# Kernel tuning notes

Hardware: AMD Instinct MI355X
Metric: run time of the kernel (lower is better)

## Reference

```python
import jax, jax.numpy as jnp
import numpy as np

INPUT, HIDDEN, Z = 64, 256, 32


def setup_inputs() -> dict:
    key = jax.random.key(0)
    ks = jax.random.split(key, 16)
    B, T = 256, 1024
    s = lambda fan_in: 1.0 / np.sqrt(fan_in)
    u = lambda k, shape, b: jax.random.uniform(k, shape, jnp.float32, -b, b)
    return {
        "x": jax.random.normal(ks[0], (B, T, INPUT), jnp.float32),
        "eps": jax.random.normal(ks[1], (T, B, Z), jnp.float32),
        # encoder q(z|x,h): Linear(hidden+input -> z)
        "enc_mu_W": u(ks[2], (Z, HIDDEN + INPUT), s(HIDDEN + INPUT)),
        "enc_mu_b": u(ks[3], (Z,), s(HIDDEN + INPUT)),
        "enc_sigma_W": u(ks[4], (Z, HIDDEN + INPUT), s(HIDDEN + INPUT)),
        "enc_sigma_b": u(ks[5], (Z,), s(HIDDEN + INPUT)),
        # prior p(z|h): Linear(hidden -> z) (computed but unused, as in source)
        "prior_mu_W": u(ks[6], (Z, HIDDEN), s(HIDDEN)),
        "prior_mu_b": u(ks[7], (Z,), s(HIDDEN)),
        "prior_sigma_W": u(ks[8], (Z, HIDDEN), s(HIDDEN)),
        "prior_sigma_b": u(ks[9], (Z,), s(HIDDEN)),
        # GRU(input+z -> hidden), torch layout: [3H, in], gates order r,z,n
        "W_ih": u(ks[10], (3 * HIDDEN, INPUT + Z), s(HIDDEN)),
        "W_hh": u(ks[11], (3 * HIDDEN, HIDDEN), s(HIDDEN)),
        "b_ih": u(ks[12], (3 * HIDDEN,), s(HIDDEN)),
        "b_hh": u(ks[13], (3 * HIDDEN,), s(HIDDEN)),
    }


def _vrnn(x, eps, enc_mu_W, enc_mu_b, enc_sigma_W, enc_sigma_b,
          prior_mu_W, prior_mu_b, prior_sigma_W, prior_sigma_b,
          W_ih, W_hh, b_ih, b_hh):
    B = x.shape[0]
    x_t_first = jnp.transpose(x, (1, 0, 2))  # [T, B, input]
    h0 = jnp.zeros((B, HIDDEN), x.dtype)

    def step(h, inp):
        x_t, eps_t = inp
        # prior (dead code in source, kept for parity; DCE'd by XLA)
        _p_mu = h @ prior_mu_W.T + prior_mu_b
        _p_lv = h @ prior_sigma_W.T + prior_sigma_b
        enc_in = jnp.concatenate([x_t, h], axis=1)  # [B, input+hidden]
        z_mu = enc_in @ enc_mu_W.T + enc_mu_b
        z_logvar = enc_in @ enc_sigma_W.T + enc_sigma_b
        z_t = z_mu + eps_t * jnp.exp(0.5 * z_logvar)
        gru_in = jnp.concatenate([x_t, z_t], axis=1)  # [B, input+z]
        gi = gru_in @ W_ih.T + b_ih  # [B, 3H]
        gh = h @ W_hh.T + b_hh       # [B, 3H]
        i_r, i_z, i_n = jnp.split(gi, 3, axis=1)
        h_r, h_z, h_n = jnp.split(gh, 3, axis=1)
        r = jax.nn.sigmoid(i_r + h_r)
        u = jax.nn.sigmoid(i_z + h_z)
        n = jnp.tanh(i_n + r * h_n)
        h_new = (1.0 - u) * n + u * h
        return h_new, None

    h_last, _ = jax.lax.scan(step, h0, (x_t_first, eps))
    return h_last  # [B, hidden]


def reference(x, eps, enc_mu_W, enc_mu_b, enc_sigma_W, enc_sigma_b,
              prior_mu_W, prior_mu_b, prior_sigma_W, prior_sigma_b,
              W_ih, W_hh, b_ih, b_hh):
    return _vrnn(x, eps, enc_mu_W, enc_mu_b, enc_sigma_W, enc_sigma_b,
                 prior_mu_W, prior_mu_b, prior_sigma_W, prior_sigma_b,
                 W_ih, W_hh, b_ih, b_hh)
```

## Files before the change

### kernel.cpp

```cpp
#include <hip/hip_runtime.h>
#include <stdint.h>

#define NB 256
#define TSEQ 1024
#define TT_MAX 64

#define REG_P 16
#define LDS_P 24
#define LDSTR 76

typedef _Float16 f16;
typedef _Float16 h2 __attribute__((ext_vector_type(2)));

static __device__ __forceinline__ uint32_t pkh2(float a, float b) {
  h2 v; v[0] = (f16)a; v[1] = (f16)b;
  return __builtin_bit_cast(uint32_t, v);
}

#if __has_builtin(__builtin_amdgcn_fdot2)
static __device__ __forceinline__ float dot2u(uint32_t w, uint32_t h, float c) {
  return __builtin_amdgcn_fdot2(__builtin_bit_cast(h2, w), __builtin_bit_cast(h2, h), c, false);
}
#else
static __device__ __forceinline__ float dot2u(uint32_t w, uint32_t h, float c) {
  h2 a = __builtin_bit_cast(h2, w), b = __builtin_bit_cast(h2, h);
  return c + (float)a[0] * (float)b[0] + (float)a[1] * (float)b[1];
}
#endif

#if __has_builtin(__builtin_amdgcn_rcpf)
#define RCPF(x) __builtin_amdgcn_rcpf(x)
#else
#define RCPF(x) (1.0f / (x))
#endif

static __device__ __forceinline__ float sigm(float x) {
  return RCPF(1.0f + exp2f(-1.44269504f * x));
}
static __device__ __forceinline__ float tanh_f(float x) {
  return 1.0f - 2.0f * RCPF(1.0f + exp2f(2.88539008f * x));
}

__global__ __launch_bounds__(512) void vrnn_pack(
    const float* __restrict__ W_hh, const float* __restrict__ W_ih,
    const float* __restrict__ emW, const float* __restrict__ esW,
    uint32_t* __restrict__ whr, uint32_t* __restrict__ whl,
    uint32_t* __restrict__ whs, uint32_t* __restrict__ whz,
    uint32_t* __restrict__ wep)
{
  const int t = threadIdx.x;
  const int r = t >> 1, q = t & 1;
  for (int rr = 0; rr < 3; ++rr) {
    const float* R = W_hh + (size_t)(r + rr * 256) * 256 + q * 128;
    for (int cj = 0; cj < 4; ++cj)
      for (int i = 0; i < 4; ++i) {
        int p = cj * 4 + i;
        whr[(((size_t)rr * 4 + cj) * 512 + t) * 4 + i] = pkh2(R[2 * p], R[2 * p + 1]);
      }
    for (int p = 0; p < LDS_P; ++p)
      whl[(size_t)t * LDSTR + rr * LDS_P + p] = pkh2(R[2 * (p + REG_P)], R[2 * (p + REG_P) + 1]);
    for (int m = 0; m < 3; ++m)
      for (int k = 0; k < 2; ++k)
        for (int i = 0; i < 4; ++i) {
          int p = (10 + 2 * m + k) * 4 + i;
          whs[(((size_t)m * 6 + rr * 2 + k) * 512 + t) * 4 + i] = pkh2(R[2 * p], R[2 * p + 1]);
        }
    const float* Z = W_ih + (size_t)(r + rr * 256) * 96 + 64 + q * 16;
    for (int cj = 0; cj < 2; ++cj)
      for (int i = 0; i < 4; ++i) {
        int p = cj * 4 + i;
        whz[(((size_t)rr * 2 + cj) * 512 + t) * 4 + i] = pkh2(Z[2 * p], Z[2 * p + 1]);
      }
  }
  {
    const int e = t & 63, s = t >> 6;
    const float* esrc = (e < 32) ? (emW + (size_t)e * 320 + 64)
                                 : (esW + (size_t)(e - 32) * 320 + 64);
    for (int p4 = 0; p4 < 4; ++p4)
      for (int i = 0; i < 4; ++i) {
        int pc = s * 16 + p4 * 4 + i;
        wep[((size_t)p4 * 512 + t) * 4 + i] = pkh2(esrc[2 * pc], esrc[2 * pc + 1]);
      }
  }
}

__global__ __launch_bounds__(256, 2) void vrnn_pre(
    const float* __restrict__ x, const float* __restrict__ W_ih,
    const float* __restrict__ b_ih, const float* __restrict__ b_hh,
    const float* __restrict__ emW, const float* __restrict__ emb,
    const float* __restrict__ esW, const float* __restrict__ esb,
    f16* __restrict__ gix, f16* __restrict__ zx,
    int chunk_t0, int TT, int nTT)
{
  const int tid = threadIdx.x;
  const int b  = blockIdx.x / nTT;
  const int tt = blockIdx.x % nTT;
  const int tloc0 = tt * TT;

  uint32_t wx[3][32];
  float bias[3];
  #pragma unroll
  for (int rr = 0; rr < 3; ++rr) {
    int j = tid + rr * 256;
    const float4* wr = (const float4*)(W_ih + (size_t)j * 96);
    #pragma unroll
    for (int p4 = 0; p4 < 16; ++p4) {
      float4 v = wr[p4];
      wx[rr][2 * p4]     = pkh2(v.x, v.y);
      wx[rr][2 * p4 + 1] = pkh2(v.z, v.w);
    }
    bias[rr] = b_ih[j] + (rr < 2 ? b_hh[j] : 0.0f);
  }
  uint32_t we[32]; float ebias = 0.0f;
  if (tid < 64) {
    const float* src = (tid < 32) ? (emW + (size_t)tid * 320)
                                  : (esW + (size_t)(tid - 32) * 320);
    #pragma unroll
    for (int p = 0; p < 32; ++p) we[p] = pkh2(src[2 * p], src[2 * p + 1]);
    ebias = (tid < 32) ? emb[tid] : esb[tid - 32];
  }

  __shared__ uint32_t xs[TT_MAX * 32];
  for (int idx = tid; idx < TT * 32; idx += 256) {
    int tl = idx >> 5, pk = idx & 31;
    size_t base = ((size_t)b * TSEQ + (chunk_t0 + tloc0 + tl)) * 64 + 2 * pk;
    xs[idx] = pkh2(x[base], x[base + 1]);
  }
  __syncthreads();

  for (int tl = 0; tl < TT; ++tl) {
    float a0 = bias[0], a1 = bias[1], a2 = bias[2];
    #pragma unroll
    for (int p = 0; p < 32; ++p) {
      uint32_t u = xs[tl * 32 + p];
      a0 = dot2u(wx[0][p], u, a0);
      a1 = dot2u(wx[1][p], u, a1);
      a2 = dot2u(wx[2][p], u, a2);
    }
    size_t ob = (size_t)(tloc0 + tl) * NB + b;
    f16* g = gix + ob * 768;
    g[tid] = (f16)a0; g[tid + 256] = (f16)a1; g[tid + 512] = (f16)a2;
    if (tid < 64) {
      float a3 = ebias;
      #pragma unroll
      for (int p = 0; p < 32; ++p) a3 = dot2u(we[p], xs[tl * 32 + p], a3);
      zx[ob * 64 + tid] = (f16)a3;
    }
  }
}

__global__ __launch_bounds__(512) void vrnn_rec(
    const f16* __restrict__ gix, const f16* __restrict__ zx,
    const float* __restrict__ eps,
    const uint32_t* __restrict__ whr, const uint32_t* __restrict__ whl_g,
    const uint32_t* __restrict__ whs, const uint32_t* __restrict__ whz,
    const uint32_t* __restrict__ wep_g,
    const float* __restrict__ b_hh,
    float* __restrict__ hws, float* __restrict__ out,
    int t0, int Tlen, int first, int last)
{
  const int t = threadIdx.x;
  const int b = blockIdx.x;
  const int r = t >> 1, q = t & 1;

  uint32_t wrg[3][REG_P];
  {
    const uint4* w4 = (const uint4*)whr;
    #pragma unroll
    for (int c = 0; c < 12; ++c) {
      uint4 v = w4[c * 512 + t];
      int rr = c >> 2, p4 = c & 3;
      wrg[rr][4 * p4] = v.x; wrg[rr][4 * p4 + 1] = v.y;
      wrg[rr][4 * p4 + 2] = v.z; wrg[rr][4 * p4 + 3] = v.w;
    }
  }
  uint32_t wz[3][8];
  {
    const uint4* w4 = (const uint4*)whz;
    #pragma unroll
    for (int c = 0; c < 6; ++c) {
      uint4 v = w4[c * 512 + t];
      int rr = c >> 1, p4 = c & 1;
      wz[rr][4 * p4] = v.x; wz[rr][4 * p4 + 1] = v.y;
      wz[rr][4 * p4 + 2] = v.z; wz[rr][4 * p4 + 3] = v.w;
    }
  }
  uint32_t we[16];
  {
    const uint4* w4 = (const uint4*)wep_g;
    #pragma unroll
    for (int c = 0; c < 4; ++c) {
      uint4 v = w4[c * 512 + t];
      we[4 * c] = v.x; we[4 * c + 1] = v.y; we[4 * c + 2] = v.z; we[4 * c + 3] = v.w;
    }
  }
  #pragma unroll
  for (int rr = 0; rr < 3; ++rr) {
    #pragma unroll
    for (int i = 0; i < REG_P; ++i) asm volatile("" : "+v"(wrg[rr][i]));
    #pragma unroll
    for (int i = 0; i < 8; ++i)    asm volatile("" : "+v"(wz[rr][i]));
  }
  #pragma unroll
  for (int i = 0; i < 16; ++i) asm volatile("" : "+v"(we[i]));
  const float bhn = b_hh[512 + r];

  __shared__ uint32_t lwh[512 * LDSTR];
  __shared__ __align__(16) f16 hf[2][264];
  __shared__ float encp[512];
  __shared__ uint32_t zu[16];

  {
    const uint4* src = (const uint4*)(whl_g + (size_t)t * LDSTR);
    uint4* dst = (uint4*)(lwh + (size_t)t * LDSTR);
    #pragma unroll
    for (int j = 0; j < LDSTR / 4; ++j) dst[j] = src[j];
  }

  const int hwidx = r + ((r >> 7) << 3);
  float hm = 0.0f;
  if (!q) {
    hm = first ? 0.0f : hws[b * 256 + r];
    hf[0][hwidx] = (f16)hm;
  }
  __syncthreads();

  float pf_g0 = 0.0f, pf_g1 = 0.0f, pf_g2 = 0.0f;
  if (!q) {
    const f16* gp0 = gix + (size_t)b * 768;
    pf_g0 = (float)gp0[r]; pf_g1 = (float)gp0[r + 256]; pf_g2 = (float)gp0[r + 512];
  }
  float pf_zm = 0.0f, pf_zl = 0.0f, pf_ep = 0.0f;
  if (t < 32) {
    const f16* zp = zx + (size_t)b * 64;
    pf_zm = (float)zp[t]; pf_zl = (float)zp[32 + t];
    pf_ep = eps[((size_t)t0 * NB + b) * 32 + t];
  }

  const int s = t >> 6;
  const int abase = 4 * s + (s >= 4 ? 1 : 0);
  const int bq = q ? 17 : 0;
  const uint32_t* myl = lwh + (size_t)t * LDSTR;
  const uint4* whs4 = (const uint4*)whs;

  uint4 sbuf[6];
  #pragma unroll
  for (int j = 0; j < 6; ++j) sbuf[j] = whs4[j * 512 + t];
  __builtin_amdgcn_sched_barrier(0);

  for (int tl = 0; tl < Tlen; ++tl) {
    const int cur = tl & 1, nxt = cur ^ 1;
    const uint4* hu4 = (const uint4*)&hf[cur][0];

    float ep_ = 0.0f;
    #pragma unroll
    for (int p4 = 0; p4 < 4; ++p4) {
      uint4 u4 = hu4[abase + p4];
      ep_ = dot2u(we[4 * p4],     u4.x, ep_);
      ep_ = dot2u(we[4 * p4 + 1], u4.y, ep_);
      ep_ = dot2u(we[4 * p4 + 2], u4.z, ep_);
      ep_ = dot2u(we[4 * p4 + 3], u4.w, ep_);
    }
    encp[t] = ep_;
    __syncthreads();

    if (t < 32) {
      float mu = pf_zm, lv = pf_zl;
      #pragma unroll
      for (int ss = 0; ss < 8; ++ss) {
        mu += encp[ss * 64 + t];
        lv += encp[ss * 64 + 32 + t];
      }
      float z = mu + pf_ep * exp2f(0.72134752f * lv);
      ((f16*)zu)[t] = (f16)z;
    }
    float g0 = 0.0f, g1 = 0.0f, g2 = 0.0f;
    #pragma unroll
    for (int g4 = 0; g4 < 4; ++g4) {
      uint4 u4 = hu4[bq + g4];
      g0 = dot2u(wrg[0][4 * g4],     u4.x, g0);
      g1 = dot2u(wrg[1][4 * g4],     u4.x, g1);
      g2 = dot2u(wrg[2][4 * g4],     u4.x, g2);
      g0 = dot2u(wrg[0][4 * g4 + 1], u4.y, g0);
      g1 = dot2u(wrg[1][4 * g4 + 1], u4.y, g1);
      g2 = dot2u(wrg[2][4 * g4 + 1], u4.y, g2);
      g0 = dot2u(wrg[0][4 * g4 + 2], u4.z, g0);
      g1 = dot2u(wrg[1][4 * g4 + 2], u4.z, g1);
      g2 = dot2u(wrg[2][4 * g4 + 2], u4.z, g2);
      g0 = dot2u(wrg[0][4 * g4 + 3], u4.w, g0);
      g1 = dot2u(wrg[1][4 * g4 + 3], u4.w, g1);
      g2 = dot2u(wrg[2][4 * g4 + 3], u4.w, g2);
    }
    {
      uint4 hq0 = hu4[bq + 10], hq1 = hu4[bq + 11];
      g0 = dot2u(sbuf[0].x, hq0.x, g0); g0 = dot2u(sbuf[0].y, hq0.y, g0);
      g0 = dot2u(sbuf[0].z, hq0.z, g0); g0 = dot2u(sbuf[0].w, hq0.w, g0);
      g1 = dot2u(sbuf[2].x, hq0.x, g1); g1 = dot2u(sbuf[2].y, hq0.y, g1);
      g1 = dot2u(sbuf[2].z, hq0.z, g1); g1 = dot2u(sbuf[2].w, hq0.w, g1);
      g2 = dot2u(sbuf[4].x, hq0.x, g2); g2 = dot2u(sbuf[4].y, hq0.y, g2);
      g2 = dot2u(sbuf[4].z, hq0.z, g2); g2 = dot2u(sbuf[4].w, hq0.w, g2);
      g0 = dot2u(sbuf[1].x, hq1.x, g0); g0 = dot2u(sbuf[1].y, hq1.y, g0);
      g0 = dot2u(sbuf[1].z, hq1.z, g0); g0 = dot2u(sbuf[1].w, hq1.w, g0);
      g1 = dot2u(sbuf[3].x, hq1.x, g1); g1 = dot2u(sbuf[3].y, hq1.y, g1);
      g1 = dot2u(sbuf[3].z, hq1.z, g1); g1 = dot2u(sbuf[3].w, hq1.w, g1);
      g2 = dot2u(sbuf[5].x, hq1.x, g2); g2 = dot2u(sbuf[5].y, hq1.y, g2);
      g2 = dot2u(sbuf[5].z, hq1.z, g2); g2 = dot2u(sbuf[5].w, hq1.w, g2);
    }
    #pragma unroll
    for (int j = 0; j < 6; ++j) sbuf[j] = whs4[(6 + j) * 512 + t];
    __builtin_amdgcn_sched_barrier(0);
    #pragma unroll
    for (int g4 = 0; g4 < 3; ++g4) {
      uint4 u4 = hu4[bq + 4 + g4];
      uint4 w0 = *(const uint4*)(myl + 0 * LDS_P + 4 * g4);
      uint4 w1 = *(const uint4*)(myl + 1 * LDS_P + 4 * g4);
      uint4 w2 = *(const uint4*)(myl + 2 * LDS_P + 4 * g4);
      g0 = dot2u(w0.x, u4.x, g0); g1 = dot2u(w1.x, u4.x, g1); g2 = dot2u(w2.x, u4.x, g2);
      g0 = dot2u(w0.y, u4.y, g0); g1 = dot2u(w1.y, u4.y, g1); g2 = dot2u(w2.y, u4.y, g2);
      g0 = dot2u(w0.z, u4.z, g0); g1 = dot2u(w1.z, u4.z, g1); g2 = dot2u(w2.z, u4.z, g2);
      g0 = dot2u(w0.w, u4.w, g0); g1 = dot2u(w1.w, u4.w, g1); g2 = dot2u(w2.w, u4.w, g2);
    }
    {
      uint4 hq0 = hu4[bq + 12], hq1 = hu4[bq + 13];
      g0 = dot2u(sbuf[0].x, hq0.x, g0); g0 = dot2u(sbuf[0].y, hq0.y, g0);
      g0 = dot2u(sbuf[0].z, hq0.z, g0); g0 = dot2u(sbuf[0].w, hq0.w, g0);
      g1 = dot2u(sbuf[2].x, hq0.x, g1); g1 = dot2u(sbuf[2].y, hq0.y, g1);
      g1 = dot2u(sbuf[2].z, hq0.z, g1); g1 = dot2u(sbuf[2].w, hq0.w, g1);
      g2 = dot2u(sbuf[4].x, hq0.x, g2); g2 = dot2u(sbuf[4].y, hq0.y, g2);
      g2 = dot2u(sbuf[4].z, hq0.z, g2); g2 = dot2u(sbuf[4].w, hq0.w, g2);
      g0 = dot2u(sbuf[1].x, hq1.x, g0); g0 = dot2u(sbuf[1].y, hq1.y, g0);
      g0 = dot2u(sbuf[1].z, hq1.z, g0); g0 = dot2u(sbuf[1].w, hq1.w, g0);
      g1 = dot2u(sbuf[3].x, hq1.x, g1); g1 = dot2u(sbuf[3].y, hq1.y, g1);
      g1 = dot2u(sbuf[3].z, hq1.z, g1); g1 = dot2u(sbuf[3].w, hq1.w, g1);
      g2 = dot2u(sbuf[5].x, hq1.x, g2); g2 = dot2u(sbuf[5].y, hq1.y, g2);
      g2 = dot2u(sbuf[5].z, hq1.z, g2); g2 = dot2u(sbuf[5].w, hq1.w, g2);
    }
    #pragma unroll
    for (int j = 0; j < 6; ++j) sbuf[j] = whs4[(12 + j) * 512 + t];
    __builtin_amdgcn_sched_barrier(0);
    #pragma unroll
    for (int g4 = 3; g4 < 6; ++g4) {
      uint4 u4 = hu4[bq + 4 + g4];
      uint4 w0 = *(const uint4*)(myl + 0 * LDS_P + 4 * g4);
      uint4 w1 = *(const uint4*)(myl + 1 * LDS_P + 4 * g4);
      uint4 w2 = *(const uint4*)(myl + 2 * LDS_P + 4 * g4);
      g0 = dot2u(w0.x, u4.x, g0); g1 = dot2u(w1.x, u4.x, g1); g2 = dot2u(w2.x, u4.x, g2);
      g0 = dot2u(w0.y, u4.y, g0); g1 = dot2u(w1.y, u4.y, g1); g2 = dot2u(w2.y, u4.y, g2);
      g0 = dot2u(w0.z, u4.z, g0); g1 = dot2u(w1.z, u4.z, g1); g2 = dot2u(w2.z, u4.z, g2);
      g0 = dot2u(w0.w, u4.w, g0); g1 = dot2u(w1.w, u4.w, g1); g2 = dot2u(w2.w, u4.w, g2);
    }
    {
      uint4 hq0 = hu4[bq + 14], hq1 = hu4[bq + 15];
      g0 = dot2u(sbuf[0].x, hq0.x, g0); g0 = dot2u(sbuf[0].y, hq0.y, g0);
      g0 = dot2u(sbuf[0].z, hq0.z, g0); g0 = dot2u(sbuf[0].w, hq0.w, g0);
      g1 = dot2u(sbuf[2].x, hq0.x, g1); g1 = dot2u(sbuf[2].y, hq0.y, g1);
      g1 = dot2u(sbuf[2].z, hq0.z, g1); g1 = dot2u(sbuf[2].w, hq0.w, g1);
      g2 = dot2u(sbuf[4].x, hq0.x, g2); g2 = dot2u(sbuf[4].y, hq0.y, g2);
      g2 = dot2u(sbuf[4].z, hq0.z, g2); g2 = dot2u(sbuf[4].w, hq0.w, g2);
      g0 = dot2u(sbuf[1].x, hq1.x, g0); g0 = dot2u(sbuf[1].y, hq1.y, g0);
      g0 = dot2u(sbuf[1].z, hq1.z, g0); g0 = dot2u(sbuf[1].w, hq1.w, g0);
      g1 = dot2u(sbuf[3].x, hq1.x, g1); g1 = dot2u(sbuf[3].y, hq1.y, g1);
      g1 = dot2u(sbuf[3].z, hq1.z, g1); g1 = dot2u(sbuf[3].w, hq1.w, g1);
      g2 = dot2u(sbuf[5].x, hq1.x, g2); g2 = dot2u(sbuf[5].y, hq1.y, g2);
      g2 = dot2u(sbuf[5].z, hq1.z, g2); g2 = dot2u(sbuf[5].w, hq1.w, g2);
    }
    __syncthreads();

    float q0 = 0.0f, q1 = 0.0f, q2 = 0.0f;
    #pragma unroll
    for (int p = 0; p < 8; ++p) {
      uint32_t u = zu[q * 8 + p];
      q0 = dot2u(wz[0][p], u, q0);
      q1 = dot2u(wz[1][p], u, q1);
      q2 = dot2u(wz[2][p], u, q2);
    }
    g0 += __shfl_xor(g0, 1); g1 += __shfl_xor(g1, 1); g2 += __shfl_xor(g2, 1);
    q0 += __shfl_xor(q0, 1); q1 += __shfl_xor(q1, 1); q2 += __shfl_xor(q2, 1);
    if (!q) {
      float rg = sigm(pf_g0 + g0 + q0);
      float uu = sigm(pf_g1 + g1 + q1);
      float n  = tanh_f(pf_g2 + q2 + rg * (g2 + bhn));
      hm = (1.0f - uu) * n + uu * hm;
      hf[nxt][hwidx] = (f16)hm;
    }

    #pragma unroll
    for (int j = 0; j < 6; ++j) sbuf[j] = whs4[j * 512 + t];
    __builtin_amdgcn_sched_barrier(0);

    int tn = (tl + 1 < Tlen) ? tl + 1 : tl;
    if (!q) {
      const f16* gp = gix + ((size_t)tn * NB + b) * 768;
      pf_g0 = (float)gp[r]; pf_g1 = (float)gp[r + 256]; pf_g2 = (float)gp[r + 512];
    }
    if (t < 32) {
      const f16* zp = zx + ((size_t)tn * NB + b) * 64;
      pf_zm = (float)zp[t]; pf_zl = (float)zp[32 + t];
      pf_ep = eps[((size_t)(t0 + tn) * NB + b) * 32 + t];
    }
    __syncthreads();
  }

  if (!q) {
    if (last) out[b * 256 + r] = hm;
    else      hws[b * 256 + r] = hm;
  }
}

extern "C" void kernel_launch(void* const* d_in, const int* in_sizes, int n_in,
                              void* d_out, int out_size, void* d_ws, size_t ws_size,
                              hipStream_t stream) {
  const float* x    = (const float*)d_in[0];
  const float* eps  = (const float*)d_in[1];
  const float* emW  = (const float*)d_in[2];
  const float* emb  = (const float*)d_in[3];
  const float* esW  = (const float*)d_in[4];
  const float* esb  = (const float*)d_in[5];
  const float* W_ih = (const float*)d_in[10];
  const float* W_hh = (const float*)d_in[11];
  const float* b_ih = (const float*)d_in[12];
  const float* b_hh = (const float*)d_in[13];
  float* out = (float*)d_out;

  const size_t o_whr = 262144;
  const size_t o_whl = o_whr + 98304;
  const size_t o_whs = o_whl + 155648;
  const size_t o_whz = o_whs + 147456;
  const size_t o_wep = o_whz + 49152;
  const size_t o_gix = o_wep + 32768;
  int Tc = TSEQ;
  while (Tc > 8 && o_gix + (size_t)Tc * NB * (768 + 64) * 2 > ws_size) Tc >>= 1;

  float*    hws   = (float*)d_ws;
  uint32_t* whr   = (uint32_t*)((char*)d_ws + o_whr);
  uint32_t* whl_g = (uint32_t*)((char*)d_ws + o_whl);
  uint32_t* whs   = (uint32_t*)((char*)d_ws + o_whs);
  uint32_t* whz   = (uint32_t*)((char*)d_ws + o_whz);
  uint32_t* wep   = (uint32_t*)((char*)d_ws + o_wep);
  f16*      gix   = (f16*)((char*)d_ws + o_gix);
  f16*      zx    = gix + (size_t)Tc * NB * 768;

  vrnn_pack<<<dim3(1), dim3(512), 0, stream>>>(W_hh, W_ih, emW, esW,
                                               whr, whl_g, whs, whz, wep);

  int nch = TSEQ / Tc;
  int TT  = Tc < 64 ? Tc : 64;
  int nTT = Tc / TT;

  for (int c = 0; c < nch; ++c) {
    vrnn_pre<<<dim3(NB * nTT), dim3(256), 0, stream>>>(
        x, W_ih, b_ih, b_hh, emW, emb, esW, esb, gix, zx, c * Tc, TT, nTT);
    vrnn_rec<<<dim3(NB), dim3(512), 0, stream>>>(
        gix, zx, eps, whr, whl_g, whs, whz, wep, b_hh, hws, out,
        c * Tc, Tc, c == 0 ? 1 : 0, c == nch - 1 ? 1 : 0);
  }
}
```

Measured before the change: 2.534 ms.

## Reduce encoder partial sums with wave shuffles instead of LDS and barrier

Remaps the encoder weight layout so each group of 8 lanes holds the 8 k-slices of one latent's mu row, and the adjacent 8 lanes hold the same latent's logvar row. The partial dot products are then reduced with xor shuffles inside the wave, which removes the encp shared buffer and one __syncthreads per timestep from the sequential recurrence. The h-chunk reads are rotated per lane to spread LDS bank access. In exchange it adds shuffle instructions, and the z computation is now spread over 32 lanes across all waves instead of the first 32 threads.

```diff
diff --git a/kernel.cpp b/kernel.cpp
--- a/kernel.cpp
+++ b/kernel.cpp
@@ -73,14 +73,20 @@
       }
   }
   {
-    const int e = t & 63, s = t >> 6;
-    const float* esrc = (e < 32) ? (emW + (size_t)e * 320 + 64)
-                                 : (esW + (size_t)(e - 32) * 320 + 64);
-    for (int p4 = 0; p4 < 4; ++p4)
+    const int l = t & 63, w = t >> 6;
+    const int e = 4 * w + (l >> 4);
+    const int role = (l >> 3) & 1;
+    const int ks = l & 7;
+    const int row = role ? (32 + e) : e;
+    const float* esrc = (row < 32) ? (emW + (size_t)row * 320 + 64)
+                                   : (esW + (size_t)(row - 32) * 320 + 64);
+    for (int j = 0; j < 4; ++j) {
+      int jp = (j + ks) & 3;
       for (int i = 0; i < 4; ++i) {
-        int pc = s * 16 + p4 * 4 + i;
-        wep[((size_t)p4 * 512 + t) * 4 + i] = pkh2(esrc[2 * pc], esrc[2 * pc + 1]);
+        int pc = ks * 16 + jp * 4 + i;
+        wep[((size_t)j * 512 + t) * 4 + i] = pkh2(esrc[2 * pc], esrc[2 * pc + 1]);
       }
+    }
   }
 }
 
@@ -207,7 +213,6 @@
 
   __shared__ uint32_t lwh[512 * LDSTR];
   __shared__ __align__(16) f16 hf[2][264];
-  __shared__ float encp[512];
   __shared__ uint32_t zu[16];
 
   {
@@ -225,20 +230,24 @@
   }
   __syncthreads();
 
+  const int lA  = t & 63;
+  const int ksA = lA & 7;
+  const int hbA = 4 * ksA + (ksA >= 4 ? 1 : 0);
+  const int zlane = ((t & 15) == 0);
+  const int ze    = 4 * (t >> 6) + ((t >> 4) & 3);
+
   float pf_g0 = 0.0f, pf_g1 = 0.0f, pf_g2 = 0.0f;
   if (!q) {
     const f16* gp0 = gix + (size_t)b * 768;
     pf_g0 = (float)gp0[r]; pf_g1 = (float)gp0[r + 256]; pf_g2 = (float)gp0[r + 512];
   }
   float pf_zm = 0.0f, pf_zl = 0.0f, pf_ep = 0.0f;
-  if (t < 32) {
+  if (zlane) {
     const f16* zp = zx + (size_t)b * 64;
-    pf_zm = (float)zp[t]; pf_zl = (float)zp[32 + t];
-    pf_ep = eps[((size_t)t0 * NB + b) * 32 + t];
-  }
-
-  const int s = t >> 6;
-  const int abase = 4 * s + (s >= 4 ? 1 : 0);
+    pf_zm = (float)zp[ze]; pf_zl = (float)zp[32 + ze];
+    pf_ep = eps[((size_t)t0 * NB + b) * 32 + ze];
+  }
+
   const int bq = q ? 17 : 0;
   const uint32_t* myl = lwh + (size_t)t * LDSTR;
   const uint4* whs4 = (const uint4*)whs;
@@ -252,28 +261,26 @@
     const int cur = tl & 1, nxt = cur ^ 1;
     const uint4* hu4 = (const uint4*)&hf[cur][0];
 
-    float ep_ = 0.0f;
-    #pragma unroll
-    for (int p4 = 0; p4 < 4; ++p4) {
-      uint4 u4 = hu4[abase + p4];
-      ep_ = dot2u(we[4 * p4],     u4.x, ep_);
-      ep_ = dot2u(we[4 * p4 + 1], u4.y, ep_);
-      ep_ = dot2u(we[4 * p4 + 2], u4.z, ep_);
-      ep_ = dot2u(we[4 * p4 + 3], u4.w, ep_);
-    }
-    encp[t] = ep_;
-    __syncthreads();
-
-    if (t < 32) {
-      float mu = pf_zm, lv = pf_zl;
+    {
+      float ep = 0.0f;
       #pragma unroll
-      for (int ss = 0; ss < 8; ++ss) {
-        mu += encp[ss * 64 + t];
-        lv += encp[ss * 64 + 32 + t];
+      for (int j = 0; j < 4; ++j) {
+        uint4 u4 = hu4[hbA + ((j + ksA) & 3)];
+        ep = dot2u(we[4 * j],     u4.x, ep);
+        ep = dot2u(we[4 * j + 1], u4.y, ep);
+        ep = dot2u(we[4 * j + 2], u4.z, ep);
+        ep = dot2u(we[4 * j + 3], u4.w, ep);
       }
-      float z = mu + pf_ep * exp2f(0.72134752f * lv);
-      ((f16*)zu)[t] = (f16)z;
-    }
+      ep += __shfl_xor(ep, 1);
+      ep += __shfl_xor(ep, 2);
+      ep += __shfl_xor(ep, 4);
+      float other = __shfl_xor(ep, 8);
+      if (zlane) {
+        float z = (pf_zm + ep) + pf_ep * exp2f(0.72134752f * (pf_zl + other));
+        ((f16*)zu)[ze] = (f16)z;
+      }
+    }
+
     float g0 = 0.0f, g1 = 0.0f, g2 = 0.0f;
     #pragma unroll
     for (int g4 = 0; g4 < 4; ++g4) {
@@ -393,10 +400,10 @@
       const f16* gp = gix + ((size_t)tn * NB + b) * 768;
       pf_g0 = (float)gp[r]; pf_g1 = (float)gp[r + 256]; pf_g2 = (float)gp[r + 512];
     }
-    if (t < 32) {
+    if (zlane) {
       const f16* zp = zx + ((size_t)tn * NB + b) * 64;
-      pf_zm = (float)zp[t]; pf_zl = (float)zp[32 + t];
-      pf_ep = eps[((size_t)(t0 + tn) * NB + b) * 32 + t];
+      pf_zm = (float)zp[ze]; pf_zl = (float)zp[32 + ze];
+      pf_ep = eps[((size_t)(t0 + tn) * NB + b) * 32 + ze];
     }
     __syncthreads();
   }
```

New measurement: 2.768 ms. +9.2%, slower.
